# Kernel tuning notes

Hardware: AMD Instinct MI355X
Metric: run time of the kernel (lower is better)

Reference implementation:

```python
import jax, jax.numpy as jnp
import numpy as np

KERNEL_MUL = 2.0
KERNEL_NUM = 5
EPS = 1e-06


def setup_inputs() -> dict:
    key = jax.random.key(0)
    k1, k2 = jax.random.split(key)
    N, D = 4096, 256
    source = jax.random.normal(k1, (N, D), dtype=jnp.float32)
    target = jax.random.normal(k2, (N, D), dtype=jnp.float32)
    return {"source": source, "target": target}


def reference(source, target):
    n_src = source.shape[0]
    total = jnp.concatenate([source, target], axis=0)  # [2N, D]
    n = total.shape[0]
    # the broadcasted (total0 - total1)**2 sum, without the O(N^2*D) tensor).
    sq = jnp.sum(total * total, axis=1)  # [2N]
    L2 = sq[:, None] + sq[None, :] - 2.0 * (total @ total.T)  # [2N, 2N]
    # Bandwidth from detached distances (torch uses L2_distance.data).
    bandwidth = jax.lax.stop_gradient(jnp.sum(L2)) / (n * n - n)
    bandwidth = bandwidth / (KERNEL_MUL ** (KERNEL_NUM // 2))
    kernels = jnp.zeros_like(L2)
    for i in range(KERNEL_NUM):
        bw = bandwidth * (KERNEL_MUL ** i)
        kernels = kernels + jnp.exp(-L2 / (bw + EPS))
    XX = kernels[:n_src, :n_src]
    YY = kernels[n_src:, n_src:]
    XY = kernels[:n_src, n_src:]
    YX = kernels[n_src:, :n_src]
    return jnp.mean(XX + YY - XY - YX)
```

## Files before the change

### kernel.cpp

```cpp
#include <hip/hip_runtime.h>

#define N_TOT 8192
#define NS 4096
#define D 256
#define NB 64
#define NTRI (NB*(NB+1)/2)
#define HALF_B 32

typedef float f32x16 __attribute__((ext_vector_type(16)));
typedef float f32x2 __attribute__((ext_vector_type(2)));
typedef short bf16x8 __attribute__((ext_vector_type(8)));

__device__ __forceinline__ void gload16(const void* g, void* l) {
  __builtin_amdgcn_global_load_lds(
      (const __attribute__((address_space(1))) unsigned int*)g,
      (__attribute__((address_space(3))) unsigned int*)l,
      16, 0, 0);
}

__device__ __forceinline__ unsigned short f2bf(float f) {
  unsigned int u = __builtin_bit_cast(unsigned int, f);
  u += 0x7FFFu + ((u >> 16) & 1u);
  return (unsigned short)(u >> 16);
}

__global__ void k_prep(const float* __restrict__ src, const float* __restrict__ tgt,
                       unsigned short* __restrict__ Xb, float* __restrict__ sqv,
                       float* __restrict__ pm, float* __restrict__ wsqp) {
  __shared__ float colacc[256];
  __shared__ float wred[4];
  int t = threadIdx.x, l = t & 63, w = t >> 6;
  colacc[t] = 0.f;
  __syncthreads();
  int base = blockIdx.x * 32;
  float c0 = 0.f, c1 = 0.f, c2 = 0.f, c3 = 0.f;
  float wsq = 0.f;
  #pragma unroll
  for (int r = 0; r < 8; ++r) {
    int row = base + w * 8 + r;
    const float* p = (row < NS) ? (src + (size_t)row * D) : (tgt + (size_t)(row - NS) * D);
    float4 v = ((const float4*)p)[l];
    ushort4 bv;
    bv.x = f2bf(v.x); bv.y = f2bf(v.y); bv.z = f2bf(v.z); bv.w = f2bf(v.w);
    ((ushort4*)(Xb + (size_t)row * D))[l] = bv;
    c0 += v.x; c1 += v.y; c2 += v.z; c3 += v.w;
    float s = fmaf(v.x, v.x, fmaf(v.y, v.y, fmaf(v.z, v.z, v.w * v.w)));
    for (int o = 32; o > 0; o >>= 1) s += __shfl_down(s, o, 64);
    if (l == 0) { sqv[row] = s; wsq += s; }
  }
  atomicAdd(&colacc[4 * l + 0], c0);
  atomicAdd(&colacc[4 * l + 1], c1);
  atomicAdd(&colacc[4 * l + 2], c2);
  atomicAdd(&colacc[4 * l + 3], c3);
  if (l == 0) wred[w] = wsq;
  __syncthreads();
  pm[blockIdx.x * 256 + t] = colacc[t];
  if (t == 0) wsqp[blockIdx.x] = (wred[0] + wred[1]) + (wred[2] + wred[3]);
}

__global__ void k_bw(const float* __restrict__ pm, const float* __restrict__ wsqp,
                     float* __restrict__ coef) {
  __shared__ double red[256];
  int t = threadIdx.x;
  float cs = 0.f;
  for (int b = 0; b < 256; ++b) cs += pm[b * 256 + t];
  red[t] = (double)cs * (double)cs;
  __syncthreads();
  for (int s = 128; s > 0; s >>= 1) {
    if (t < s) red[t] += red[t + s];
    __syncthreads();
  }
  double msq = red[0];
  __syncthreads();
  red[t] = (double)wsqp[t];
  __syncthreads();
  for (int s = 128; s > 0; s >>= 1) {
    if (t < s) red[t] += red[t + s];
    __syncthreads();
  }
  if (t == 0) {
    double Sv = red[0];
    double n = (double)N_TOT;
    double sumL2 = 2.0 * n * Sv - 2.0 * msq;
    double bw = sumL2 / (n * n - n) / 4.0;
    double c4 = 1.0 / (bw * 16.0 + 1e-6);
    coef[0] = (float)(c4 * 1.4426950408889634);
  }
}

__global__ __launch_bounds__(256) void k_main(
    const unsigned short* __restrict__ Xb, const float* __restrict__ sqv,
    const float* __restrict__ coef, float* __restrict__ bpart) {
  int b = blockIdx.x;
  int bi = (int)((2.f * NB + 1.f - sqrtf((float)((2 * NB + 1) * (2 * NB + 1) - 8 * b))) * 0.5f);
  if (bi < 0) bi = 0;
  if (bi > NB - 1) bi = NB - 1;
  while ((bi + 1) * (2 * NB - bi) / 2 <= b) ++bi;
  while (bi * (2 * NB - bi + 1) / 2 > b) --bi;
  int bj = bi + (b - bi * (2 * NB - bi + 1) / 2);

  __shared__ unsigned short ldsA[128 * 64];
  __shared__ unsigned short ldsB[128 * 64];
  __shared__ float sqA[128], sqB[128];
  __shared__ float redw[4];

  int t = threadIdx.x, l = t & 63, w = t >> 6;
  int lr = l & 31, half = l >> 5;
  int waveRow = w >> 1, waveCol = w & 1;

  if (t < 128) sqA[t] = sqv[bi * 128 + t];
  else         sqB[t - 128] = sqv[bj * 128 + (t - 128)];
  float A4 = coef[0];

  const unsigned short* arow = Xb + (size_t)bi * 128 * D;
  const unsigned short* brow = Xb + (size_t)bj * 128 * D;

  f32x16 acc[2][2] = {};

  for (int ko = 0; ko < 4; ++ko) {
    if (ko) __syncthreads();
    int kOff = ko * 64;
    #pragma unroll
    for (int p = 0; p < 4; ++p) {
      int seg = p * 256 + w * 64 + l;
      int row = seg >> 3;
      int kb = (seg & 7) ^ (row & 7) ^ ((row >> 3) & 7);
      int goff = row * D + kOff + kb * 8;
      gload16(arow + goff, &ldsA[(p * 4 + w) * 512]);
      gload16(brow + goff, &ldsB[(p * 4 + w) * 512]);
    }
    __syncthreads();
    #pragma unroll
    for (int ks = 0; ks < 4; ++ks) {
      int c = 2 * ks + half;
      bf16x8 aF[2], bF[2];
      #pragma unroll
      for (int rb = 0; rb < 2; ++rb) {
        int rowA = waveRow * 64 + rb * 32 + lr;
        int physA = c ^ (rowA & 7) ^ ((rowA >> 3) & 7);
        aF[rb] = *(const bf16x8*)&ldsA[rowA * 64 + physA * 8];
        int rowB = waveCol * 64 + rb * 32 + lr;
        int physB = c ^ (rowB & 7) ^ ((rowB >> 3) & 7);
        bF[rb] = *(const bf16x8*)&ldsB[rowB * 64 + physB * 8];
      }
      #pragma unroll
      for (int rb = 0; rb < 2; ++rb)
        #pragma unroll
        for (int cb = 0; cb < 2; ++cb)
          acc[rb][cb] = __builtin_amdgcn_mfma_f32_32x32x16_bf16(aF[rb], bF[cb], acc[rb][cb], 0, 0, 0);
    }
  }

  float c2A4 = 2.f * A4, nA4 = -A4;
  f32x2 lsum2 = {0.f, 0.f};
  bool diag = (bi == bj);
  #pragma unroll
  for (int cb = 0; cb < 2; ++cb) {
    int jj = waveCol * 64 + cb * 32 + lr;
    float bjv = nA4 * sqB[jj];
    #pragma unroll
    for (int rb = 0; rb < 2; ++rb) {
      #pragma unroll
      for (int r = 0; r < 16; r += 2) {
        int ii = waveRow * 64 + rb * 32 + (r & 3) + 8 * (r >> 2) + 4 * half;
        f32x2 dot2 = {acc[rb][cb][r], acc[rb][cb][r + 1]};
        f32x2 sq2 = {sqA[ii], sqA[ii + 1]};
        f32x2 tt = c2A4 * dot2 + (nA4 * sq2 + bjv);
        f32x2 e;
        e.x = __builtin_amdgcn_exp2f(tt.x);
        e.y = __builtin_amdgcn_exp2f(tt.y);
        f32x2 e2 = e * e, e4 = e2 * e2, e8 = e4 * e4, e16 = e8 * e8;
        f32x2 kern = ((e + e2) + (e4 + e8)) + e16;
        if (diag) {
          if (ii == jj) kern.x = 0.f;
          if (ii + 1 == jj) kern.y = 0.f;
        }
        lsum2 += kern;
      }
    }
  }
  float lsum = lsum2.x + lsum2.y;
  for (int o = 32; o > 0; o >>= 1) lsum += __shfl_down(lsum, o, 64);
  if (l == 0) redw[w] = lsum;
  __syncthreads();
  if (t == 0) {
    float tot = (redw[0] + redw[1]) + (redw[2] + redw[3]);
    float wgt = diag ? 1.f : 2.f;
    float sgn = ((bi < HALF_B) == (bj < HALF_B)) ? 1.f : -1.f;
    bpart[b] = tot * wgt * sgn;
  }
}

__global__ void k_final(const float* __restrict__ bpart, float* __restrict__ out) {
  __shared__ double red[256];
  int t = threadIdx.x;
  double s = 0.0;
  for (int k = 0; k < 9; ++k) {
    int idx = k * 256 + t;
    if (idx < NTRI) s += (double)bpart[idx];
  }
  red[t] = s;
  __syncthreads();
  for (int st = 128; st > 0; st >>= 1) {
    if (t < st) red[t] += red[t + st];
    __syncthreads();
  }
  if (t == 0) {
    double total = red[0] + 5.0 * (double)N_TOT;
    out[0] = (float)(total / ((double)NS * (double)NS));
  }
}

extern "C" void kernel_launch(void* const* d_in, const int* in_sizes, int n_in,
                              void* d_out, int out_size, void* d_ws, size_t ws_size,
                              hipStream_t stream) {
  const float* src = (const float*)d_in[0];
  const float* tgt = (const float*)d_in[1];
  float* out = (float*)d_out;
  char* ws = (char*)d_ws;
  unsigned short* Xb = (unsigned short*)ws;
  float* sqv  = (float*)(ws + (4u << 20));
  float* pm   = (float*)(ws + (4u << 20) + (32u << 10));
  float* wsqp = (float*)(ws + (4u << 20) + (288u << 10));
  float* coef = (float*)(ws + (4u << 20) + (289u << 10));
  float* bpart = (float*)(ws + (4u << 20) + (290u << 10));

  hipLaunchKernelGGL(k_prep, dim3(256), dim3(256), 0, stream, src, tgt, Xb, sqv, pm, wsqp);
  hipLaunchKernelGGL(k_bw, dim3(1), dim3(256), 0, stream, pm, wsqp, coef);
  hipLaunchKernelGGL(k_main, dim3(NTRI), dim3(256), 0, stream, Xb, sqv, coef, bpart);
  hipLaunchKernelGGL(k_final, dim3(1), dim3(256), 0, stream, bpart, out);
}
```

Measured before the change: 107.2 us.

## Use 256x128 rectangular tiles with 512-thread blocks over the upper triangle

Replaces the 128x128 triangular tile enumeration with 256-row by 128-column tiles covering the upper triangle. Each block now runs 8 waves, and each wave owns one 32-row strip across four column blocks. Tiles that straddle the diagonal mask the elements on or below it, and every tile is weighted by two. The aim is more reuse of the A tile in LDS, a more even load balance, and fewer blocks. The cost is more LDS per block and masking work that is partly wasted on straddling tiles.

```diff
diff --git a/kernel.cpp b/kernel.cpp
--- a/kernel.cpp
+++ b/kernel.cpp
@@ -3,8 +3,9 @@
 #define N_TOT 8192
 #define NS 4096
 #define D 256
-#define NB 64
-#define NTRI (NB*(NB+1)/2)
+#define NIP 32
+#define NJP 64
+#define NTILE 1056
 #define HALF_B 32
 
 typedef float f32x16 __attribute__((ext_vector_type(16)));
@@ -88,95 +89,92 @@
   }
 }
 
-__global__ __launch_bounds__(256) void k_main(
+__global__ __launch_bounds__(512, 4) void k_main(
     const unsigned short* __restrict__ Xb, const float* __restrict__ sqv,
     const float* __restrict__ coef, float* __restrict__ bpart) {
   int b = blockIdx.x;
-  int bi = (int)((2.f * NB + 1.f - sqrtf((float)((2 * NB + 1) * (2 * NB + 1) - 8 * b))) * 0.5f);
-  if (bi < 0) bi = 0;
-  if (bi > NB - 1) bi = NB - 1;
-  while ((bi + 1) * (2 * NB - bi) / 2 <= b) ++bi;
-  while (bi * (2 * NB - bi + 1) / 2 > b) --bi;
-  int bj = bi + (b - bi * (2 * NB - bi + 1) / 2);
-
-  __shared__ unsigned short ldsA[128 * 64];
+  int I = (int)((65.f - sqrtf(65.f * 65.f - 4.f * (float)b)) * 0.5f);
+  if (I < 0) I = 0;
+  if (I > NIP - 1) I = NIP - 1;
+  while (I * (65 - I) > b) --I;
+  while ((I + 1) * (65 - (I + 1)) <= b) ++I;
+  int J = 2 * I + (b - I * (65 - I));
+
+  __shared__ unsigned short ldsA[256 * 64];
   __shared__ unsigned short ldsB[128 * 64];
-  __shared__ float sqA[128], sqB[128];
-  __shared__ float redw[4];
+  __shared__ float sqA[256], sqB[128];
+  __shared__ float redw[8];
 
   int t = threadIdx.x, l = t & 63, w = t >> 6;
   int lr = l & 31, half = l >> 5;
-  int waveRow = w >> 1, waveCol = w & 1;
-
-  if (t < 128) sqA[t] = sqv[bi * 128 + t];
-  else         sqB[t - 128] = sqv[bj * 128 + (t - 128)];
+
   float A4 = coef[0];
-
-  const unsigned short* arow = Xb + (size_t)bi * 128 * D;
-  const unsigned short* brow = Xb + (size_t)bj * 128 * D;
-
-  f32x16 acc[2][2] = {};
+  if (t < 256)      sqA[t] = sqv[I * 256 + t];
+  else if (t < 384) sqB[t - 256] = sqv[J * 128 + (t - 256)];
+
+  const unsigned short* arow = Xb + (size_t)I * 256 * D;
+  const unsigned short* brow = Xb + (size_t)J * 128 * D;
+
+  f32x16 acc[4] = {};
 
   for (int ko = 0; ko < 4; ++ko) {
     if (ko) __syncthreads();
     int kOff = ko * 64;
     #pragma unroll
     for (int p = 0; p < 4; ++p) {
-      int seg = p * 256 + w * 64 + l;
+      int seg = p * 512 + t;
       int row = seg >> 3;
       int kb = (seg & 7) ^ (row & 7) ^ ((row >> 3) & 7);
-      int goff = row * D + kOff + kb * 8;
-      gload16(arow + goff, &ldsA[(p * 4 + w) * 512]);
-      gload16(brow + goff, &ldsB[(p * 4 + w) * 512]);
+      gload16(arow + row * D + kOff + kb * 8, &ldsA[(p * 512 + w * 64) * 8]);
+    }
+    #pragma unroll
+    for (int p = 0; p < 2; ++p) {
+      int seg = p * 512 + t;
+      int row = seg >> 3;
+      int kb = (seg & 7) ^ (row & 7) ^ ((row >> 3) & 7);
+      gload16(brow + row * D + kOff + kb * 8, &ldsB[(p * 512 + w * 64) * 8]);
     }
     __syncthreads();
     #pragma unroll
     for (int ks = 0; ks < 4; ++ks) {
       int c = 2 * ks + half;
-      bf16x8 aF[2], bF[2];
+      int rowA = 32 * w + lr;
+      int physA = c ^ (rowA & 7) ^ ((rowA >> 3) & 7);
+      bf16x8 aF = *(const bf16x8*)&ldsA[rowA * 64 + physA * 8];
       #pragma unroll
-      for (int rb = 0; rb < 2; ++rb) {
-        int rowA = waveRow * 64 + rb * 32 + lr;
-        int physA = c ^ (rowA & 7) ^ ((rowA >> 3) & 7);
-        aF[rb] = *(const bf16x8*)&ldsA[rowA * 64 + physA * 8];
-        int rowB = waveCol * 64 + rb * 32 + lr;
+      for (int cb = 0; cb < 4; ++cb) {
+        int rowB = 32 * cb + lr;
         int physB = c ^ (rowB & 7) ^ ((rowB >> 3) & 7);
-        bF[rb] = *(const bf16x8*)&ldsB[rowB * 64 + physB * 8];
+        bf16x8 bF = *(const bf16x8*)&ldsB[rowB * 64 + physB * 8];
+        acc[cb] = __builtin_amdgcn_mfma_f32_32x32x16_bf16(aF, bF, acc[cb], 0, 0, 0);
       }
-      #pragma unroll
-      for (int rb = 0; rb < 2; ++rb)
-        #pragma unroll
-        for (int cb = 0; cb < 2; ++cb)
-          acc[rb][cb] = __builtin_amdgcn_mfma_f32_32x32x16_bf16(aF[rb], bF[cb], acc[rb][cb], 0, 0, 0);
     }
   }
 
   float c2A4 = 2.f * A4, nA4 = -A4;
   f32x2 lsum2 = {0.f, 0.f};
-  bool diag = (bi == bj);
+  bool straddle = ((J >> 1) == I);
+  int dj = 128 * (J - 2 * I);
   #pragma unroll
-  for (int cb = 0; cb < 2; ++cb) {
-    int jj = waveCol * 64 + cb * 32 + lr;
+  for (int cb = 0; cb < 4; ++cb) {
+    int jj = 32 * cb + lr;
     float bjv = nA4 * sqB[jj];
     #pragma unroll
-    for (int rb = 0; rb < 2; ++rb) {
-      #pragma unroll
-      for (int r = 0; r < 16; r += 2) {
-        int ii = waveRow * 64 + rb * 32 + (r & 3) + 8 * (r >> 2) + 4 * half;
-        f32x2 dot2 = {acc[rb][cb][r], acc[rb][cb][r + 1]};
-        f32x2 sq2 = {sqA[ii], sqA[ii + 1]};
-        f32x2 tt = c2A4 * dot2 + (nA4 * sq2 + bjv);
-        f32x2 e;
-        e.x = __builtin_amdgcn_exp2f(tt.x);
-        e.y = __builtin_amdgcn_exp2f(tt.y);
-        f32x2 e2 = e * e, e4 = e2 * e2, e8 = e4 * e4, e16 = e8 * e8;
-        f32x2 kern = ((e + e2) + (e4 + e8)) + e16;
-        if (diag) {
-          if (ii == jj) kern.x = 0.f;
-          if (ii + 1 == jj) kern.y = 0.f;
-        }
-        lsum2 += kern;
+    for (int r = 0; r < 16; r += 2) {
+      int ii = 32 * w + (r & 3) + 8 * (r >> 2) + 4 * half;
+      f32x2 dot2 = {acc[cb][r], acc[cb][r + 1]};
+      f32x2 sq2 = {sqA[ii], sqA[ii + 1]};
+      f32x2 tt = c2A4 * dot2 + (nA4 * sq2 + bjv);
+      f32x2 e;
+      e.x = __builtin_amdgcn_exp2f(tt.x);
+      e.y = __builtin_amdgcn_exp2f(tt.y);
+      f32x2 e2 = e * e, e4 = e2 * e2, e8 = e4 * e4, e16 = e8 * e8;
+      f32x2 kern = ((e + e2) + (e4 + e8)) + e16;
+      if (straddle) {
+        if (jj + dj <= ii) kern.x = 0.f;
+        if (jj + dj <= ii + 1) kern.y = 0.f;
       }
+      lsum2 += kern;
     }
   }
   float lsum = lsum2.x + lsum2.y;
@@ -184,10 +182,10 @@
   if (l == 0) redw[w] = lsum;
   __syncthreads();
   if (t == 0) {
-    float tot = (redw[0] + redw[1]) + (redw[2] + redw[3]);
-    float wgt = diag ? 1.f : 2.f;
-    float sgn = ((bi < HALF_B) == (bj < HALF_B)) ? 1.f : -1.f;
-    bpart[b] = tot * wgt * sgn;
+    float tot = ((redw[0] + redw[1]) + (redw[2] + redw[3])) +
+                ((redw[4] + redw[5]) + (redw[6] + redw[7]));
+    float sgn = ((I < 16) == (J < 32)) ? 1.f : -1.f;
+    bpart[b] = tot * 2.f * sgn;
   }
 }
 
@@ -195,9 +193,9 @@
   __shared__ double red[256];
   int t = threadIdx.x;
   double s = 0.0;
-  for (int k = 0; k < 9; ++k) {
+  for (int k = 0; k < 5; ++k) {
     int idx = k * 256 + t;
-    if (idx < NTRI) s += (double)bpart[idx];
+    if (idx < NTILE) s += (double)bpart[idx];
   }
   red[t] = s;
   __syncthreads();
@@ -227,6 +225,6 @@
 
   hipLaunchKernelGGL(k_prep, dim3(256), dim3(256), 0, stream, src, tgt, Xb, sqv, pm, wsqp);
   hipLaunchKernelGGL(k_bw, dim3(1), dim3(256), 0, stream, pm, wsqp, coef);
-  hipLaunchKernelGGL(k_main, dim3(NTRI), dim3(256), 0, stream, Xb, sqv, coef, bpart);
+  hipLaunchKernelGGL(k_main, dim3(NTILE), dim3(512), 0, stream, Xb, sqv, coef, bpart);
   hipLaunchKernelGGL(k_final, dim3(1), dim3(256), 0, stream, bpart, out);
 }
```

New measurement: 109.3 us. About the same (+2.0%).
